# Performance work log

Measured on AMD Instinct MI355X. Metric: run time of the kernel, lower is better.

Reference implementation:

```python
import jax, jax.numpy as jnp
import numpy as np

V, E, H = 1024, 32, 64
D = 8                     # number of tree levels (root at depth 0)
PER = 149796              # nodes per non-root level
N = 1 + 7 * PER           # 1048573 total nodes


def setup_inputs() -> dict:
    rng = np.random.default_rng(0)
    sizes = [1] + [PER] * (D - 1)
    off = np.concatenate([[0], np.cumsum(sizes)])
    depth = np.repeat(np.arange(D), sizes).astype(np.int64)
    parent = np.zeros(N, dtype=np.int64)  # root points to itself (harmless: its h is 0 when read)
    for l in range(1, D):
        parent[off[l]:off[l + 1]] = rng.integers(off[l - 1], off[l], sizes[l])
    token_ids = rng.integers(0, V, N).astype(np.int64)

    key = jax.random.key(0)
    ks = jax.random.split(key, 7)
    s = 0.05
    return {
        "token_ids": jnp.asarray(token_ids),
        "parent": jnp.asarray(parent),
        "depth": jnp.asarray(depth),
        "max_depth": D - 1,
        "emb": jax.random.normal(ks[0], (V, E), jnp.float32) * s,
        "W_iou_w": jax.random.normal(ks[1], (3 * H, E), jnp.float32) * s,
        "W_iou_b": jax.random.normal(ks[2], (3 * H,), jnp.float32) * s,
        "U_iou_w": jax.random.normal(ks[3], (3 * H, H), jnp.float32) * s,
        "W_f_w": jax.random.normal(ks[4], (H, E), jnp.float32) * s,
        "W_f_b": jax.random.normal(ks[5], (H,), jnp.float32) * s,
        "U_f_w": jax.random.normal(ks[6], (H, H), jnp.float32) * s,
    }


def reference(token_ids, parent, depth, max_depth, emb,
              W_iou_w, W_iou_b, U_iou_w, W_f_w, W_f_b, U_f_w):
    n = token_ids.shape[0]
    hid = U_f_w.shape[0]
    x = emb[token_ids]                                 # [N, E]
    wiou_x = x @ W_iou_w.T + W_iou_b                   # [N, 3H] (input part, precomputed)
    wf_x = x @ W_f_w.T + W_f_b                         # [N, H]
    h = jnp.zeros((n, hid), x.dtype)
    c = jnp.zeros((n, hid), x.dtype)
    # level-synchronous bottom-up sweep (deepest level first); children of a
    # depth-d node are exactly at depth d+1, already finalized when d is processed
    for d in range(max_depth, -1, -1):
        h_sum = jax.ops.segment_sum(h, parent, num_segments=n)        # child-sum per parent
        f = jax.nn.sigmoid(wf_x[parent] + h @ U_f_w.T)                # forget gate per child edge
        fc = jax.ops.segment_sum(f * c, parent, num_segments=n)      # sum_k f_k * c_k per parent
        iou = wiou_x + h_sum @ U_iou_w.T
        i, o, u = jnp.split(iou, 3, axis=-1)
        c_new = jax.nn.sigmoid(i) * jnp.tanh(u) + fc
        h_new = jax.nn.sigmoid(o) * jnp.tanh(c_new)
        m = (depth == d)[:, None]
        h = jnp.where(m, h_new, h)
        c = jnp.where(m, c_new, c)
    return h[0]  # root hidden state, matching TreeLSTMEncoder.forward
```

## Files before the change

kernel.cpp:

```cpp
#include <hip/hip_runtime.h>
#include <hip/hip_fp16.h>
#include <string.h>

#define PER  149796
#define NN   1048573
#define HDIM 64
#define EDIM 32
#define NIOU 192

typedef _Float16 f16;
typedef _Float16 f16x8 __attribute__((ext_vector_type(8)));
typedef _Float16 f16x2 __attribute__((ext_vector_type(2)));
typedef float    f32x4 __attribute__((ext_vector_type(4)));

__device__ __forceinline__ float sigf(float x){ return 1.0f/(1.0f+__expf(-x)); }
__device__ __forceinline__ float tanh_f(float x){
  float ax = fabsf(x);
  float e  = __expf(-2.0f*ax);
  float t  = (1.0f - e)/(1.0f + e);
  return x < 0.0f ? -t : t;
}

__device__ __forceinline__ void atomAddH2(f16x2* p, f16 a, f16 b){
#if defined(__HIP_DEVICE_COMPILE__)
  typedef _Float16 h2 __attribute__((ext_vector_type(2)));
  h2 v; v[0]=a; v[1]=b;
  (void)__builtin_amdgcn_global_atomic_fadd_v2f16(
      (__attribute__((address_space(1))) h2*)p, v);
#else
  (void)p; (void)a; (void)b;
#endif
}

__global__ __launch_bounds__(256) void tablepack_kernel(
    const float* __restrict__ emb, const float* __restrict__ Wiou, const float* __restrict__ biou,
    const float* __restrict__ Wf, const float* __restrict__ bf,
    const float* __restrict__ Uf, const float* __restrict__ Uiou,
    float* __restrict__ embWiou, float* __restrict__ embWf,
    f16* __restrict__ Bfp, f16* __restrict__ Biop)
{
  if (blockIdx.x < 1024){
    int v = blockIdx.x;
    int m = threadIdx.x;
    const float* x = emb + (size_t)v*EDIM;
    if (m < NIOU){
      float a = biou[m];
      #pragma unroll
      for (int e=0;e<EDIM;e++) a += Wiou[m*EDIM+e]*x[e];
      embWiou[(size_t)v*NIOU + m] = a;
    } else {
      int mm = m - NIOU;
      float a = bf[mm];
      #pragma unroll
      for (int e=0;e<EDIM;e++) a += Wf[mm*EDIM+e]*x[e];
      embWf[(size_t)v*HDIM + mm] = a;
    }
  } else {
    for (int i = threadIdx.x; i < 2*4*64*8; i += 256){
      int j = i & 7, L = (i>>3)&63, st = i>>9;
      int t = st & 3, s = st >> 2;
      int k = s*32 + (L>>4)*8 + j;
      int n = t*16 + (L&15);
      Bfp[i] = (f16)Uf[n*HDIM + k];
    }
    for (int i = threadIdx.x; i < 2*12*64*8; i += 256){
      int j = i & 7, L = (i>>3)&63, st = i>>9;
      int t = st % 12, s = st / 12;
      int k = s*32 + (L>>4)*8 + j;
      int n = t*16 + (L&15);
      Biop[i] = (f16)Uiou[n*HDIM + k];
    }
  }
}

__global__ __launch_bounds__(64,4) void level_kernel(
    const int* __restrict__ tok, const int* __restrict__ parent,
    const float* __restrict__ embWiou, const float* __restrict__ embWf,
    const f16* __restrict__ Biopack, const f16* __restrict__ Ufpack,
    const f16x2* __restrict__ accIn, f16x2* __restrict__ accOut,
    int poff, int ppoff, int mode)
{
  __shared__ f16 Ah[16*72];
  __shared__ f16 FAf[16*68];
  int lane = threadIdx.x;
  int j0   = blockIdx.x*16;
  int q = lane>>4, c16 = lane&15;

  if (mode != 0){
    #pragma unroll
    for (int i=0;i<16;i++){
      int j = j0 + i; if (j > PER-1) j = PER-1;
      f16x2 v = accIn[(size_t)j*HDIM + lane];
      Ah[i*72 + lane]  = v.x;
      FAf[i*68 + lane] = v.y;
    }
  } else {
    #pragma unroll
    for (int i=0;i<16;i++){
      Ah[i*72 + lane]  = (f16)0.f;
      FAf[i*68 + lane] = (f16)0.f;
    }
  }
  __syncthreads();
  f16x8 A0 = *(const f16x8*)(Ah + c16*72 + q*8);
  f16x8 A1 = *(const f16x8*)(Ah + c16*72 + 32 + q*8);

  const f16x8* Bp = (const f16x8*)Biopack;
  f32x4 acc[12];
  #pragma unroll
  for (int nt=0;nt<12;nt++) acc[nt] = (f32x4){0.f,0.f,0.f,0.f};
  #pragma unroll
  for (int nt=0;nt<12;nt++){
    f16x8 B0 = Bp[nt*64 + lane];
    f16x8 B1 = Bp[(12+nt)*64 + lane];
    acc[nt] = __builtin_amdgcn_mfma_f32_16x16x32_f16(A0, B0, acc[nt], 0,0,0);
    acc[nt] = __builtin_amdgcn_mfma_f32_16x16x32_f16(A1, B1, acc[nt], 0,0,0);
  }
  float cc[4][4];
  f16   hh[4][4];
  int   prow_[4]; int wt_[4]; bool ok_[4];
  #pragma unroll
  for (int r=0;r<4;r++){
    int j = j0 + q*4 + r;
    bool ok = j < PER;
    int jl = ok ? j : PER-1;
    int g = poff + jl;
    int tk = tok[g];
    const float* tr = embWiou + (size_t)tk*NIOU;
    ok_[r] = ok;
    if (mode != 2){
      int pg = parent[g];
      prow_[r] = pg - ppoff;
      wt_[r]   = tok[pg];
    } else {
      prow_[r] = jl;
      wt_[r]   = tok[0];
    }
    int prow = q*4 + r;
    #pragma unroll
    for (int nt=0;nt<4;nt++){
      int col = nt*16 + c16;
      float ai = acc[nt][r]   + tr[col];
      float ao = acc[nt+4][r] + tr[64+col];
      float au = acc[nt+8][r] + tr[128+col];
      float fav = (float)FAf[prow*68 + col];
      float c = sigf(ai)*tanh_f(au) + fav;
      float h = sigf(ao)*tanh_f(c);
      cc[r][nt] = c;
      hh[r][nt] = (f16)h;
    }
  }
  __syncthreads();
  #pragma unroll
  for (int r=0;r<4;r++)
    #pragma unroll
    for (int nt=0;nt<4;nt++)
      Ah[(q*4+r)*72 + nt*16 + c16] = hh[r][nt];
  __syncthreads();
  f16x8 H0 = *(const f16x8*)(Ah + c16*72 + q*8);
  f16x8 H1 = *(const f16x8*)(Ah + c16*72 + 32 + q*8);
  const f16x8* Up = (const f16x8*)Ufpack;
  f32x4 g4[4];
  #pragma unroll
  for (int nt=0;nt<4;nt++) g4[nt] = (f32x4){0.f,0.f,0.f,0.f};
  #pragma unroll
  for (int nt=0;nt<4;nt++){
    f16x8 B0 = Up[nt*64 + lane];
    f16x8 B1 = Up[(4+nt)*64 + lane];
    g4[nt] = __builtin_amdgcn_mfma_f32_16x16x32_f16(H0, B0, g4[nt], 0,0,0);
    g4[nt] = __builtin_amdgcn_mfma_f32_16x16x32_f16(H1, B1, g4[nt], 0,0,0);
  }
  #pragma unroll
  for (int r=0;r<4;r++){
    if (!ok_[r]) continue;
    const float* wr = embWf + (size_t)wt_[r]*HDIM;
    size_t rb = (size_t)prow_[r]*HDIM;
    #pragma unroll
    for (int nt=0;nt<4;nt++){
      int col = nt*16 + c16;
      float v = sigf(g4[nt][r] + wr[col]) * cc[r][nt];
      if (mode == 2){
        f16x2 o; o.x = hh[r][nt]; o.y = (f16)v;
        accOut[rb + col] = o;
      } else {
        atomAddH2(&accOut[rb + col], hh[r][nt], (f16)v);
      }
    }
  }
}

__global__ __launch_bounds__(256) void rootred_kernel(
    const f16x2* __restrict__ HFin, float* __restrict__ rootacc)
{
  int t = blockIdx.x*blockDim.x + threadIdx.x;
  int m = t & 63;
  int j0 = t >> 6;
  int jstep = (gridDim.x*blockDim.x) >> 6;
  float af=0.f, ah=0.f;
  for (int j=j0; j<PER; j+=jstep){
    f16x2 v = HFin[(size_t)j*HDIM + m];
    ah += (float)v.x;
    af += (float)v.y;
  }
  __shared__ float red[256];
  red[threadIdx.x]=af; __syncthreads();
  if (threadIdx.x < 64) atomicAdd(&rootacc[m],    red[m]+red[64+m]+red[128+m]+red[192+m]);
  __syncthreads();
  red[threadIdx.x]=ah; __syncthreads();
  if (threadIdx.x < 64) atomicAdd(&rootacc[64+m], red[m]+red[64+m]+red[128+m]+red[192+m]);
}

__global__ void rootnode_kernel(
    const int* __restrict__ tok, const float* __restrict__ emb,
    const float* __restrict__ Wiou, const float* __restrict__ biou, const float* __restrict__ Uiou,
    const float* __restrict__ rootacc, float* __restrict__ out)
{
  int m = threadIdx.x;
  if (m >= HDIM) return;
  int t = tok[0];
  float ai=biou[m], ao=biou[HDIM+m], au=biou[2*HDIM+m];
  for (int e=0;e<EDIM;e++){
    float xe = emb[(size_t)t*EDIM+e];
    ai += Wiou[(size_t)m*EDIM+e]*xe;
    ao += Wiou[(size_t)(HDIM+m)*EDIM+e]*xe;
    au += Wiou[(size_t)(2*HDIM+m)*EDIM+e]*xe;
  }
  for (int k=0;k<HDIM;k++){
    float hv = rootacc[64+k];
    ai += Uiou[(size_t)m*HDIM+k]*hv;
    ao += Uiou[(size_t)(HDIM+m)*HDIM+k]*hv;
    au += Uiou[(size_t)(2*HDIM+m)*HDIM+k]*hv;
  }
  float c = sigf(ai)*tanh_f(au) + rootacc[m];
  out[m] = sigf(ao)*tanh_f(c);
}

static inline char* alignup(char* p){
  uintptr_t u = (uintptr_t)p;
  u = (u + 255) & ~(uintptr_t)255;
  return (char*)u;
}

extern "C" void kernel_launch(void* const* d_in, const int* in_sizes, int n_in,
                              void* d_out, int out_size, void* d_ws, size_t ws_size,
                              hipStream_t stream)
{
  const int*   tok    = (const int*)d_in[0];
  const int*   parent = (const int*)d_in[1];
  const float* emb    = (const float*)d_in[4];
  const float* Wiou   = (const float*)d_in[5];
  const float* biou   = (const float*)d_in[6];
  const float* Uiou   = (const float*)d_in[7];
  const float* Wf     = (const float*)d_in[8];
  const float* bf     = (const float*)d_in[9];
  const float* Uf     = (const float*)d_in[10];
  float* out = (float*)d_out;

  char* w = (char*)d_ws;
  size_t BUF = (size_t)PER*HDIM*sizeof(f16x2);
  f16x2* bufA    = (f16x2*)w;  w = alignup(w + BUF);
  f16x2* bufB    = (f16x2*)w;  w = alignup(w + BUF);
  float* embWiou = (float*)w;  w = alignup(w + 1024*NIOU*sizeof(float));
  float* embWf   = (float*)w;  w = alignup(w + 1024*HDIM*sizeof(float));
  float* rootacc = (float*)w;  w = alignup(w + 128*sizeof(float));
  f16*   Ufpack  = (f16*)w;    w = alignup(w + 2*4*64*8*sizeof(f16));
  f16*   Biopack = (f16*)w;    w = alignup(w + 2*12*64*8*sizeof(f16));

  const int NB = (PER + 15)/16;

  (void)hipMemsetAsync(rootacc, 0, 128*sizeof(float), stream);
  tablepack_kernel<<<1025, 256, 0, stream>>>(emb, Wiou, biou, Wf, bf, Uf, Uiou,
                                             embWiou, embWf, Ufpack, Biopack);

  f16x2* accIn  = nullptr;
  f16x2* accOut = bufA;
  (void)hipMemsetAsync(bufA, 0, BUF, stream);
  level_kernel<<<NB, 64, 0, stream>>>(tok, parent, embWiou, embWf, Biopack, Ufpack,
                                      nullptr, bufA, 1 + 6*PER, 1 + 5*PER, 0);
  accIn = bufA; accOut = bufB;
  for (int d=6; d>=2; --d){
    (void)hipMemsetAsync(accOut, 0, BUF, stream);
    level_kernel<<<NB, 64, 0, stream>>>(tok, parent, embWiou, embWf, Biopack, Ufpack,
                                        accIn, accOut, 1 + (d-1)*PER, 1 + (d-2)*PER, 1);
    f16x2* t2 = accIn; accIn = accOut; accOut = t2;
  }
  level_kernel<<<NB, 64, 0, stream>>>(tok, parent, embWiou, embWf, Biopack, Ufpack,
                                      accIn, accOut, 1, 0, 2);

  rootred_kernel<<<256, 256, 0, stream>>>(accOut, rootacc);
  rootnode_kernel<<<1, 64, 0, stream>>>(tok, emb, Wiou, biou, Uiou, rootacc, out);
}
```

Before: 546.6 us.

## Fuse buffer zeroing and root reduction into level kernel; widen to 32 rows

Each level kernel now zeroes the input accumulator rows it just consumed, so that buffer can be reused as the next level's output. This replaces the per-level hipMemsetAsync calls with one upfront memset. The final level sums h and f*c inside the kernel and adds them into 256 atomic slices, which removes the separate rootred kernel and the write/read of the last buffer. Blocks now cover 32 rows in two MFMA passes instead of 16, which halves the grid and amortizes the LDS staging. The trade-offs are extra stores inside the level kernel, more LDS and registers per block, and a serial slice sum in the single-block root kernel.

```diff
diff --git a/kernel.cpp b/kernel.cpp
--- a/kernel.cpp
+++ b/kernel.cpp
@@ -7,6 +7,7 @@
 #define HDIM 64
 #define EDIM 32
 #define NIOU 192
+#define NS   256
 
 typedef _Float16 f16;
 typedef _Float16 f16x8 __attribute__((ext_vector_type(8)));
@@ -77,146 +78,159 @@
     const int* __restrict__ tok, const int* __restrict__ parent,
     const float* __restrict__ embWiou, const float* __restrict__ embWf,
     const f16* __restrict__ Biopack, const f16* __restrict__ Ufpack,
-    const f16x2* __restrict__ accIn, f16x2* __restrict__ accOut,
-    int poff, int ppoff, int mode)
+    f16x2* __restrict__ accIn, f16x2* __restrict__ accOut,
+    float* __restrict__ rootslice,
+    int poff, int ppoff, int mode, int doZero)
 {
-  __shared__ f16 Ah[16*72];
-  __shared__ f16 FAf[16*68];
+  __shared__ f16 Ah[32*72];
+  __shared__ f16 FAf[32*68];
+  __shared__ float redH[4*64];
+  __shared__ float redF[4*64];
   int lane = threadIdx.x;
-  int j0   = blockIdx.x*16;
+  int j0   = blockIdx.x*32;
   int q = lane>>4, c16 = lane&15;
 
   if (mode != 0){
     #pragma unroll
-    for (int i=0;i<16;i++){
+    for (int i=0;i<32;i++){
       int j = j0 + i; if (j > PER-1) j = PER-1;
       f16x2 v = accIn[(size_t)j*HDIM + lane];
       Ah[i*72 + lane]  = v.x;
       FAf[i*68 + lane] = v.y;
     }
+    if (doZero){
+      int rows = PER - j0; if (rows > 32) rows = 32;
+      uint4 z; z.x=0; z.y=0; z.z=0; z.w=0;
+      uint4* Z = (uint4*)(accIn + (size_t)j0*HDIM);
+      for (int i = lane; i < rows*16; i += 64) Z[i] = z;
+    }
   } else {
     #pragma unroll
-    for (int i=0;i<16;i++){
+    for (int i=0;i<32;i++){
       Ah[i*72 + lane]  = (f16)0.f;
       FAf[i*68 + lane] = (f16)0.f;
     }
   }
-  __syncthreads();
-  f16x8 A0 = *(const f16x8*)(Ah + c16*72 + q*8);
-  f16x8 A1 = *(const f16x8*)(Ah + c16*72 + 32 + q*8);
-
+
+  float sH[4] = {0.f,0.f,0.f,0.f};
+  float sF[4] = {0.f,0.f,0.f,0.f};
+  int tok0 = (mode == 2) ? tok[0] : 0;
   const f16x8* Bp = (const f16x8*)Biopack;
-  f32x4 acc[12];
-  #pragma unroll
-  for (int nt=0;nt<12;nt++) acc[nt] = (f32x4){0.f,0.f,0.f,0.f};
-  #pragma unroll
-  for (int nt=0;nt<12;nt++){
-    f16x8 B0 = Bp[nt*64 + lane];
-    f16x8 B1 = Bp[(12+nt)*64 + lane];
-    acc[nt] = __builtin_amdgcn_mfma_f32_16x16x32_f16(A0, B0, acc[nt], 0,0,0);
-    acc[nt] = __builtin_amdgcn_mfma_f32_16x16x32_f16(A1, B1, acc[nt], 0,0,0);
-  }
-  float cc[4][4];
-  f16   hh[4][4];
-  int   prow_[4]; int wt_[4]; bool ok_[4];
-  #pragma unroll
-  for (int r=0;r<4;r++){
-    int j = j0 + q*4 + r;
-    bool ok = j < PER;
-    int jl = ok ? j : PER-1;
-    int g = poff + jl;
-    int tk = tok[g];
-    const float* tr = embWiou + (size_t)tk*NIOU;
-    ok_[r] = ok;
-    if (mode != 2){
-      int pg = parent[g];
-      prow_[r] = pg - ppoff;
-      wt_[r]   = tok[pg];
-    } else {
-      prow_[r] = jl;
-      wt_[r]   = tok[0];
-    }
-    int prow = q*4 + r;
+  const f16x8* Up = (const f16x8*)Ufpack;
+
+  for (int t2=0; t2<2; ++t2){
+    int base = t2*16;
+    f16x8 A0 = *(const f16x8*)(Ah + (base+c16)*72 + q*8);
+    f16x8 A1 = *(const f16x8*)(Ah + (base+c16)*72 + 32 + q*8);
+    f32x4 acc[12];
+    #pragma unroll
+    for (int nt=0;nt<12;nt++) acc[nt] = (f32x4){0.f,0.f,0.f,0.f};
+    #pragma unroll
+    for (int nt=0;nt<12;nt++){
+      f16x8 B0 = Bp[nt*64 + lane];
+      f16x8 B1 = Bp[(12+nt)*64 + lane];
+      acc[nt] = __builtin_amdgcn_mfma_f32_16x16x32_f16(A0, B0, acc[nt], 0,0,0);
+      acc[nt] = __builtin_amdgcn_mfma_f32_16x16x32_f16(A1, B1, acc[nt], 0,0,0);
+    }
+    float cc[4][4];
+    f16   hh[4][4];
+    int   prow_[4]; int wt_[4]; bool ok_[4];
+    #pragma unroll
+    for (int r=0;r<4;r++){
+      int j = j0 + base + q*4 + r;
+      bool ok = j < PER;
+      int jl = ok ? j : PER-1;
+      int g = poff + jl;
+      int tk = tok[g];
+      const float* tr = embWiou + (size_t)tk*NIOU;
+      ok_[r] = ok;
+      if (mode != 2){
+        int pg = parent[g];
+        prow_[r] = pg - ppoff;
+        wt_[r]   = tok[pg];
+      } else {
+        prow_[r] = 0;
+        wt_[r]   = tok0;
+      }
+      int lrow = base + q*4 + r;
+      #pragma unroll
+      for (int nt=0;nt<4;nt++){
+        int col = nt*16 + c16;
+        float ai = acc[nt][r]   + tr[col];
+        float ao = acc[nt+4][r] + tr[64+col];
+        float au = acc[nt+8][r] + tr[128+col];
+        float fav = (float)FAf[lrow*68 + col];
+        float c = sigf(ai)*tanh_f(au) + fav;
+        float h = sigf(ao)*tanh_f(c);
+        cc[r][nt] = c;
+        hh[r][nt] = (f16)h;
+      }
+    }
+    #pragma unroll
+    for (int r=0;r<4;r++)
+      #pragma unroll
+      for (int nt=0;nt<4;nt++)
+        Ah[(base+q*4+r)*72 + nt*16 + c16] = hh[r][nt];
+    f16x8 H0 = *(const f16x8*)(Ah + (base+c16)*72 + q*8);
+    f16x8 H1 = *(const f16x8*)(Ah + (base+c16)*72 + 32 + q*8);
+    f32x4 g4[4];
+    #pragma unroll
+    for (int nt=0;nt<4;nt++) g4[nt] = (f32x4){0.f,0.f,0.f,0.f};
     #pragma unroll
     for (int nt=0;nt<4;nt++){
-      int col = nt*16 + c16;
-      float ai = acc[nt][r]   + tr[col];
-      float ao = acc[nt+4][r] + tr[64+col];
-      float au = acc[nt+8][r] + tr[128+col];
-      float fav = (float)FAf[prow*68 + col];
-      float c = sigf(ai)*tanh_f(au) + fav;
-      float h = sigf(ao)*tanh_f(c);
-      cc[r][nt] = c;
-      hh[r][nt] = (f16)h;
-    }
-  }
-  __syncthreads();
-  #pragma unroll
-  for (int r=0;r<4;r++)
-    #pragma unroll
-    for (int nt=0;nt<4;nt++)
-      Ah[(q*4+r)*72 + nt*16 + c16] = hh[r][nt];
-  __syncthreads();
-  f16x8 H0 = *(const f16x8*)(Ah + c16*72 + q*8);
-  f16x8 H1 = *(const f16x8*)(Ah + c16*72 + 32 + q*8);
-  const f16x8* Up = (const f16x8*)Ufpack;
-  f32x4 g4[4];
-  #pragma unroll
-  for (int nt=0;nt<4;nt++) g4[nt] = (f32x4){0.f,0.f,0.f,0.f};
-  #pragma unroll
-  for (int nt=0;nt<4;nt++){
-    f16x8 B0 = Up[nt*64 + lane];
-    f16x8 B1 = Up[(4+nt)*64 + lane];
-    g4[nt] = __builtin_amdgcn_mfma_f32_16x16x32_f16(H0, B0, g4[nt], 0,0,0);
-    g4[nt] = __builtin_amdgcn_mfma_f32_16x16x32_f16(H1, B1, g4[nt], 0,0,0);
-  }
-  #pragma unroll
-  for (int r=0;r<4;r++){
-    if (!ok_[r]) continue;
-    const float* wr = embWf + (size_t)wt_[r]*HDIM;
-    size_t rb = (size_t)prow_[r]*HDIM;
+      f16x8 B0 = Up[nt*64 + lane];
+      f16x8 B1 = Up[(4+nt)*64 + lane];
+      g4[nt] = __builtin_amdgcn_mfma_f32_16x16x32_f16(H0, B0, g4[nt], 0,0,0);
+      g4[nt] = __builtin_amdgcn_mfma_f32_16x16x32_f16(H1, B1, g4[nt], 0,0,0);
+    }
+    #pragma unroll
+    for (int r=0;r<4;r++){
+      if (!ok_[r]) continue;
+      const float* wr = embWf + (size_t)wt_[r]*HDIM;
+      size_t rb = (size_t)prow_[r]*HDIM;
+      #pragma unroll
+      for (int nt=0;nt<4;nt++){
+        int col = nt*16 + c16;
+        float v = sigf(g4[nt][r] + wr[col]) * cc[r][nt];
+        if (mode == 2){
+          sH[nt] += (float)hh[r][nt];
+          sF[nt] += v;
+        } else {
+          atomAddH2(&accOut[rb + col], hh[r][nt], (f16)v);
+        }
+      }
+    }
+  }
+
+  if (mode == 2){
     #pragma unroll
     for (int nt=0;nt<4;nt++){
-      int col = nt*16 + c16;
-      float v = sigf(g4[nt][r] + wr[col]) * cc[r][nt];
-      if (mode == 2){
-        f16x2 o; o.x = hh[r][nt]; o.y = (f16)v;
-        accOut[rb + col] = o;
-      } else {
-        atomAddH2(&accOut[rb + col], hh[r][nt], (f16)v);
-      }
-    }
-  }
-}
-
-__global__ __launch_bounds__(256) void rootred_kernel(
-    const f16x2* __restrict__ HFin, float* __restrict__ rootacc)
-{
-  int t = blockIdx.x*blockDim.x + threadIdx.x;
-  int m = t & 63;
-  int j0 = t >> 6;
-  int jstep = (gridDim.x*blockDim.x) >> 6;
-  float af=0.f, ah=0.f;
-  for (int j=j0; j<PER; j+=jstep){
-    f16x2 v = HFin[(size_t)j*HDIM + m];
-    ah += (float)v.x;
-    af += (float)v.y;
-  }
-  __shared__ float red[256];
-  red[threadIdx.x]=af; __syncthreads();
-  if (threadIdx.x < 64) atomicAdd(&rootacc[m],    red[m]+red[64+m]+red[128+m]+red[192+m]);
-  __syncthreads();
-  red[threadIdx.x]=ah; __syncthreads();
-  if (threadIdx.x < 64) atomicAdd(&rootacc[64+m], red[m]+red[64+m]+red[128+m]+red[192+m]);
+      redH[q*64 + nt*16 + c16] = sH[nt];
+      redF[q*64 + nt*16 + c16] = sF[nt];
+    }
+    float tH = redH[lane] + redH[64+lane] + redH[128+lane] + redH[192+lane];
+    float tF = redF[lane] + redF[64+lane] + redF[128+lane] + redF[192+lane];
+    int sl = blockIdx.x & (NS-1);
+    atomicAdd(&rootslice[sl*128 + 64 + lane], tH);
+    atomicAdd(&rootslice[sl*128 + lane],      tF);
+  }
 }
 
 __global__ void rootnode_kernel(
     const int* __restrict__ tok, const float* __restrict__ emb,
     const float* __restrict__ Wiou, const float* __restrict__ biou, const float* __restrict__ Uiou,
-    const float* __restrict__ rootacc, float* __restrict__ out)
+    const float* __restrict__ rootslice, float* __restrict__ out)
 {
+  __shared__ float hsh[64];
   int m = threadIdx.x;
   if (m >= HDIM) return;
+  float fcs = 0.f, hs = 0.f;
+  for (int s=0; s<NS; ++s){
+    fcs += rootslice[s*128 + m];
+    hs  += rootslice[s*128 + 64 + m];
+  }
+  hsh[m] = hs;
+  __syncthreads();
   int t = tok[0];
   float ai=biou[m], ao=biou[HDIM+m], au=biou[2*HDIM+m];
   for (int e=0;e<EDIM;e++){
@@ -226,12 +240,12 @@
     au += Wiou[(size_t)(2*HDIM+m)*EDIM+e]*xe;
   }
   for (int k=0;k<HDIM;k++){
-    float hv = rootacc[64+k];
+    float hv = hsh[k];
     ai += Uiou[(size_t)m*HDIM+k]*hv;
     ao += Uiou[(size_t)(HDIM+m)*HDIM+k]*hv;
     au += Uiou[(size_t)(2*HDIM+m)*HDIM+k]*hv;
   }
-  float c = sigf(ai)*tanh_f(au) + rootacc[m];
+  float c = sigf(ai)*tanh_f(au) + fcs;
   out[m] = sigf(ao)*tanh_f(c);
 }
 
@@ -258,35 +272,34 @@
 
   char* w = (char*)d_ws;
   size_t BUF = (size_t)PER*HDIM*sizeof(f16x2);
-  f16x2* bufA    = (f16x2*)w;  w = alignup(w + BUF);
-  f16x2* bufB    = (f16x2*)w;  w = alignup(w + BUF);
-  float* embWiou = (float*)w;  w = alignup(w + 1024*NIOU*sizeof(float));
-  float* embWf   = (float*)w;  w = alignup(w + 1024*HDIM*sizeof(float));
-  float* rootacc = (float*)w;  w = alignup(w + 128*sizeof(float));
-  f16*   Ufpack  = (f16*)w;    w = alignup(w + 2*4*64*8*sizeof(f16));
-  f16*   Biopack = (f16*)w;    w = alignup(w + 2*12*64*8*sizeof(f16));
-
-  const int NB = (PER + 15)/16;
-
-  (void)hipMemsetAsync(rootacc, 0, 128*sizeof(float), stream);
+  f16x2* bufA      = (f16x2*)w;  w = alignup(w + BUF);
+  f16x2* bufB      = (f16x2*)w;  w = alignup(w + BUF);
+  float* embWiou   = (float*)w;  w = alignup(w + 1024*NIOU*sizeof(float));
+  float* embWf     = (float*)w;  w = alignup(w + 1024*HDIM*sizeof(float));
+  float* rootslice = (float*)w;  w = alignup(w + (size_t)NS*128*sizeof(float));
+  f16*   Ufpack    = (f16*)w;    w = alignup(w + 2*4*64*8*sizeof(f16));
+  f16*   Biopack   = (f16*)w;    w = alignup(w + 2*12*64*8*sizeof(f16));
+
+  const int NBL = (PER + 31)/32;
+
+  (void)hipMemsetAsync(bufA, 0, 2*BUF, stream);
+  (void)hipMemsetAsync(rootslice, 0, (size_t)NS*128*sizeof(float), stream);
   tablepack_kernel<<<1025, 256, 0, stream>>>(emb, Wiou, biou, Wf, bf, Uf, Uiou,
                                              embWiou, embWf, Ufpack, Biopack);
 
-  f16x2* accIn  = nullptr;
-  f16x2* accOut = bufA;
-  (void)hipMemsetAsync(bufA, 0, BUF, stream);
-  level_kernel<<<NB, 64, 0, stream>>>(tok, parent, embWiou, embWf, Biopack, Ufpack,
-                                      nullptr, bufA, 1 + 6*PER, 1 + 5*PER, 0);
-  accIn = bufA; accOut = bufB;
+  level_kernel<<<NBL, 64, 0, stream>>>(tok, parent, embWiou, embWf, Biopack, Ufpack,
+                                       bufB , bufA, rootslice,
+                                       1 + 6*PER, 1 + 5*PER, 0, 0);
+  f16x2* accIn = bufA; f16x2* accOut = bufB;
   for (int d=6; d>=2; --d){
-    (void)hipMemsetAsync(accOut, 0, BUF, stream);
-    level_kernel<<<NB, 64, 0, stream>>>(tok, parent, embWiou, embWf, Biopack, Ufpack,
-                                        accIn, accOut, 1 + (d-1)*PER, 1 + (d-2)*PER, 1);
+    level_kernel<<<NBL, 64, 0, stream>>>(tok, parent, embWiou, embWf, Biopack, Ufpack,
+                                         accIn, accOut, rootslice,
+                                         1 + (d-1)*PER, 1 + (d-2)*PER, 1, (d > 2) ? 1 : 0);
     f16x2* t2 = accIn; accIn = accOut; accOut = t2;
   }
-  level_kernel<<<NB, 64, 0, stream>>>(tok, parent, embWiou, embWf, Biopack, Ufpack,
-                                      accIn, accOut, 1, 0, 2);
-
-  rootred_kernel<<<256, 256, 0, stream>>>(accOut, rootacc);
-  rootnode_kernel<<<1, 64, 0, stream>>>(tok, emb, Wiou, biou, Uiou, rootacc, out);
-}
+  level_kernel<<<NBL, 64, 0, stream>>>(tok, parent, embWiou, embWf, Biopack, Ufpack,
+                                       accIn, accOut , rootslice,
+                                       1, 0, 2, 0);
+
+  rootnode_kernel<<<1, 64, 0, stream>>>(tok, emb, Wiou, biou, Uiou, rootslice, out);
+}
```

Measured after the change: 1.125 ms. 106% more time.
